# Kernel tuning notes

Hardware: AMD Instinct MI355X
Metric: run time of the kernel (lower is better)

Reference implementation:

```python
import jax, jax.numpy as jnp
from jax import lax
import numpy as np

B, S, D, H2, V = 1024, 256, 128, 5, 50257
EPS = 1e-5


def setup_inputs() -> dict:
    key = jax.random.key(0)
    ks = jax.random.split(key, 12)
    s = 0.08  # init scale ~ 1/sqrt(D)
    return {
        "x": jax.random.randint(ks[0], (B, S), 0, V),
        "emb": jax.random.normal(ks[1], (V, D), jnp.float32) * s,
        "W_ih1": jax.random.normal(ks[2], (D, D), jnp.float32) * s,
        "b_ih1": jax.random.normal(ks[3], (D,), jnp.float32) * s,
        "W_hh1": jax.random.normal(ks[4], (D, D), jnp.float32) * s,
        "b_hh1": jax.random.normal(ks[5], (D,), jnp.float32) * s,
        "g1": jnp.ones((D,), jnp.float32),
        "be1": jnp.zeros((D,), jnp.float32),
        "W_ih2": jax.random.normal(ks[6], (H2, D), jnp.float32) * s,
        "b_ih2": jax.random.normal(ks[7], (H2,), jnp.float32) * s,
        "W_hh2": jax.random.normal(ks[8], (H2, H2), jnp.float32) * s,
        "b_hh2": jax.random.normal(ks[9], (H2,), jnp.float32) * s,
        "g2": jnp.ones((H2,), jnp.float32),
        "be2": jnp.zeros((H2,), jnp.float32),
    }


def _rnn(xproj, W_hh):
    """Vanilla tanh RNN. xproj: [B,S,H] = x @ W_ih^T + b_ih + b_hh (precomputed)."""
    h0 = jnp.zeros((xproj.shape[0], W_hh.shape[0]), xproj.dtype)

    def step(h, xt):  # xt: [B,H]
        h = jnp.tanh(xt + h @ W_hh.T)
        return h, h

    _, hs = lax.scan(step, h0, jnp.swapaxes(xproj, 0, 1))  # [S,B,H]
    return jnp.swapaxes(hs, 0, 1)  # [B,S,H]


def _ln(z, g, b):
    m = jnp.mean(z, axis=-1, keepdims=True)
    v = jnp.mean(jnp.square(z - m), axis=-1, keepdims=True)
    return (z - m) * lax.rsqrt(v + EPS) * g + b


def reference(x, emb, W_ih1, b_ih1, W_hh1, b_hh1, g1, be1,
              W_ih2, b_ih2, W_hh2, b_hh2, g2, be2):
    e = emb[x]  # [B,S,D]
    z = _rnn(e @ W_ih1.T + (b_ih1 + b_hh1), W_hh1)
    z = _ln(z, g1, be1)
    z = _rnn(z @ W_ih2.T + (b_ih2 + b_hh2), W_hh2)  # [B,S,5]
    z = _ln(z, g2, be2)
    pooled = jnp.mean(z, axis=1)  # AvgPool1d over full seq -> [B,5]
    return jax.nn.softmax(pooled, axis=1)
```

## Files before the change

### kernel.cpp

```cpp
#include <hip/hip_runtime.h>
#include <stdint.h>

#define S_LEN 256
#define DIM   128
#define EPSL  1e-5f

typedef __bf16 bf16x8 __attribute__((ext_vector_type(8)));
typedef float  f32x4  __attribute__((ext_vector_type(4)));

__device__ __forceinline__ unsigned short f2bf_bits(float f) {
  union { float f; unsigned int u; } v; v.f = f;
  unsigned int r = v.u + 0x7fffu + ((v.u >> 16) & 1u);
  return (unsigned short)(r >> 16);
}
__device__ __forceinline__ float bf2f_bits(unsigned short b) {
  union { float f; unsigned int u; } v; v.u = ((unsigned int)b) << 16; return v.f;
}
__device__ __forceinline__ unsigned f2bf_rhu(float f) {
  return (__float_as_uint(f) + 0x8000u) >> 16;
}
__device__ __forceinline__ unsigned pack_rhu(float lo, float hi) {
  return __builtin_amdgcn_perm(__float_as_uint(hi) + 0x8000u,
                               __float_as_uint(lo) + 0x8000u, 0x07060302u);
}
__device__ __forceinline__ float tanh_fast(float x) {
  float e = __expf(2.f * x);
  return 1.f - 2.f * __builtin_amdgcn_rcpf(e + 1.f);
}

template<int CTRL>
__device__ __forceinline__ float dpp_rot_add(float v) {
  int r = __builtin_amdgcn_update_dpp(0, __float_as_int(v), CTRL, 0xF, 0xF, true);
  return v + __int_as_float(r);
}
template<int CTRL>
__device__ __forceinline__ float dpp_rot_max(float v) {
  int r = __builtin_amdgcn_update_dpp(0, __float_as_int(v), CTRL, 0xF, 0xF, true);
  return fmaxf(v, __int_as_float(r));
}
__device__ __forceinline__ float dpp_sum16(float v) {
  v = dpp_rot_add<0x124>(v); v = dpp_rot_add<0x128>(v);
  v = dpp_rot_add<0x39>(v);  v = dpp_rot_add<0x4E>(v);
  return v;
}
__device__ __forceinline__ float dpp_max16(float v) {
  v = dpp_rot_max<0x124>(v); v = dpp_rot_max<0x128>(v);
  v = dpp_rot_max<0x39>(v);  v = dpp_rot_max<0x4E>(v);
  return v;
}
template<int CTRL>
__device__ __forceinline__ void red_level7(float& s, float& sq, float* d) {
  s  = dpp_rot_add<CTRL>(s);
  sq = dpp_rot_add<CTRL>(sq);
#pragma unroll
  for (int j = 0; j < 5; j++) d[j] = dpp_rot_add<CTRL>(d[j]);
}
template<int JJ>
__device__ __forceinline__ float bcast16(float v) {
  int r = __builtin_amdgcn_ds_swizzle(__float_as_int(v), (JJ << 5) | 0x10);
  return __int_as_float(r);
}

union Frag8 { unsigned short us[8]; bf16x8 v; int4 i4; };

__global__ __launch_bounds__(512, 2)
void rnn_fused(const int* __restrict__ x, const float* __restrict__ emb,
               const float* __restrict__ Wih1, const float* __restrict__ bih1,
               const float* __restrict__ Whh1, const float* __restrict__ bhh1,
               const float* __restrict__ g1, const float* __restrict__ be1,
               const float* __restrict__ Wih2, const float* __restrict__ bih2,
               const float* __restrict__ Whh2, const float* __restrict__ bhh2,
               const float* __restrict__ g2, const float* __restrict__ be2,
               float* __restrict__ out)
{
  __shared__ __align__(16) unsigned short h_bf[2][16 * 128];
  __shared__ __align__(16) unsigned short e_bf[2][16 * 128];
  __shared__ int x_tile[16 * 256];

  const int tid  = threadIdx.x;
  const int wave = tid >> 6;
  const int lane = tid & 63;
  const int r0   = blockIdx.x * 16;
  const int l15  = lane & 15;
  const int q    = lane >> 4;

  for (int i = tid; i < 16 * 256; i += 512)
    x_tile[i] = x[(size_t)(r0 + (i >> 8)) * S_LEN + (i & 255)];
  for (int i = tid; i < 16 * 128; i += 512) h_bf[1][i] = 0;

  const int n1 = wave * 16 + l15;
  const float bias1v = bih1[n1] + bhh1[n1];
  bf16x8 wh[4], wih[4];
#pragma unroll
  for (int kt = 0; kt < 4; kt++) {
    int k0 = kt * 32 + q * 8;
    Frag8 fh, fa;
#pragma unroll
    for (int j = 0; j < 8; j++) {
      fh.us[j] = f2bf_bits(Whh1[n1 * DIM + k0 + j]);
      fa.us[j] = f2bf_bits(Wih1[n1 * DIM + k0 + j]);
    }
    wh[kt] = fh.v; wih[kt] = fa.v;
  }

  const bool ln_role = (wave < 4);
  float w2g[5][8], Gs[5], Bs[5], wrow[5];
  float t2_l = 0.f, g2_l = 0.f, be2_l = 0.f, validf = 0.f;
  float h2rep[5], pool_l = 0.f;
  int myrow = 0;
  float pf[2][8];
  const int gm   = (wave & 3) * 4 + q;
  const int goct = l15;
  const int gdst = gm * 128 + ((goct ^ gm) & 15) * 8;

  if (ln_role) {
    myrow = wave * 4 + q;
    int coct = (l15 ^ myrow) & 15;
#pragma unroll
    for (int j = 0; j < 8; j++) {
      int c = coct * 8 + j;
      float gc = g1[c];
#pragma unroll
      for (int jj = 0; jj < 5; jj++) w2g[jj][j] = Wih2[jj * DIM + c] * gc;
    }
#pragma unroll
    for (int jj = 0; jj < 5; jj++) { Gs[jj] = 0.f; Bs[jj] = 0.f; }
    for (int c = 0; c < DIM; c++) {
      float gc = g1[c], bc = be1[c];
#pragma unroll
      for (int jj = 0; jj < 5; jj++) {
        float w = Wih2[jj * DIM + c];
        Gs[jj] += w * gc; Bs[jj] += w * bc;
      }
    }
    validf = (l15 < 5) ? 1.f : 0.f;
    if (l15 < 5) {
      t2_l = bih2[l15] + bhh2[l15];
      g2_l = g2[l15]; be2_l = be2[l15];
#pragma unroll
      for (int jj = 0; jj < 5; jj++) wrow[jj] = Whh2[l15 * 5 + jj];
    } else {
#pragma unroll
      for (int jj = 0; jj < 5; jj++) wrow[jj] = 0.f;
    }
#pragma unroll
    for (int jj = 0; jj < 5; jj++) h2rep[jj] = 0.f;
  }
  __syncthreads();

  if (!ln_role) {
    float ta[8], tb[8];
    { int xid = x_tile[gm * 256 + 0];
      const float* pe = emb + (size_t)xid * DIM + goct * 8;
#pragma unroll
      for (int j = 0; j < 8; j++) ta[j] = pe[j]; }
    { int xid = x_tile[gm * 256 + 1];
      const float* pe = emb + (size_t)xid * DIM + goct * 8;
#pragma unroll
      for (int j = 0; j < 8; j++) tb[j] = pe[j]; }
    { int xid = x_tile[gm * 256 + 2];
      const float* pe = emb + (size_t)xid * DIM + goct * 8;
#pragma unroll
      for (int j = 0; j < 8; j++) pf[0][j] = pe[j]; }
    { int xid = x_tile[gm * 256 + 3];
      const float* pe = emb + (size_t)xid * DIM + goct * 8;
#pragma unroll
      for (int j = 0; j < 8; j++) pf[1][j] = pe[j]; }
    Frag8 pa, pb;
#pragma unroll
    for (int j = 0; j < 8; j++) { pa.us[j] = f2bf_bits(ta[j]); pb.us[j] = f2bf_bits(tb[j]); }
    *(int4*)&e_bf[0][gdst] = pa.i4;
    *(int4*)&e_bf[1][gdst] = pb.i4;
  }
  __syncthreads();

  f32x4 xpacc = {bias1v, bias1v, bias1v, bias1v};
#pragma unroll
  for (int kt = 0; kt < 4; kt++) {
    int sw = (((kt * 4 + q) ^ l15) & 15) * 8;
    bf16x8 ae = *(const bf16x8*)&e_bf[0][l15 * 128 + sw];
    xpacc = __builtin_amdgcn_mfma_f32_16x16x32_bf16(ae, wih[kt], xpacc, 0, 0, 0);
  }
  asm volatile("s_waitcnt lgkmcnt(0)\n\ts_barrier" ::: "memory");

#pragma unroll 2
  for (int t = 0; t <= S_LEN; t++) {
    f32x4 acc = xpacc;
    if (t < S_LEN) {
      const int rb = (t + 1) & 1;
#pragma unroll
      for (int kt = 0; kt < 4; kt++) {
        int sw = (((kt * 4 + q) ^ l15) & 15) * 8;
        bf16x8 ahf = *(const bf16x8*)&h_bf[rb][l15 * 128 + sw];
        acc = __builtin_amdgcn_mfma_f32_16x16x32_bf16(ahf, wh[kt], acc, 0, 0, 0);
      }
      const int wb = t & 1;
      const int c = n1;
      const int oct = c >> 3;
#pragma unroll
      for (int r = 0; r < 4; r++) {
        int row = q * 4 + r;
        h_bf[wb][row * 128 + ((oct ^ row) & 15) * 8 + (c & 7)] =
            (unsigned short)f2bf_rhu(tanh_fast(acc[r]));
      }
    }

    if (t + 1 < S_LEN) {
      f32x4 a = {bias1v, bias1v, bias1v, bias1v};
#pragma unroll
      for (int kt = 0; kt < 4; kt++) {
        int sw = (((kt * 4 + q) ^ l15) & 15) * 8;
        bf16x8 ae = *(const bf16x8*)&e_bf[(t + 1) & 1][l15 * 128 + sw];
        a = __builtin_amdgcn_mfma_f32_16x16x32_bf16(ae, wih[kt], a, 0, 0, 0);
      }
      xpacc = a;
    }

    if (!ln_role) {
      if (t + 2 < S_LEN) {
        int4 pk;
        pk.x = pack_rhu(pf[t & 1][0], pf[t & 1][1]);
        pk.y = pack_rhu(pf[t & 1][2], pf[t & 1][3]);
        pk.z = pack_rhu(pf[t & 1][4], pf[t & 1][5]);
        pk.w = pack_rhu(pf[t & 1][6], pf[t & 1][7]);
        *(int4*)&e_bf[t & 1][gdst] = pk;
      }
      if (t + 4 < S_LEN) {
        int xid = x_tile[gm * 256 + t + 4];
        const float* pe = emb + (size_t)xid * DIM + goct * 8;
#pragma unroll
        for (int j = 0; j < 8; j++) pf[t & 1][j] = pe[j];
      }
    } else if (t >= 1) {
      const int hb = (t - 1) & 1;
      Frag8 hr;
      hr.i4 = *(const int4*)&h_bf[hb][myrow * 128 + l15 * 8];
      float s = 0.f, sq = 0.f, d[5] = {0, 0, 0, 0, 0};
#pragma unroll
      for (int j = 0; j < 8; j++) {
        float v = bf2f_bits(hr.us[j]);
        s += v; sq += v * v;
#pragma unroll
        for (int jj = 0; jj < 5; jj++) d[jj] = fmaf(w2g[jj][j], v, d[jj]);
      }
      red_level7<0x124>(s, sq, d);
      red_level7<0x128>(s, sq, d);
      red_level7<0x39>(s, sq, d);
      red_level7<0x4E>(s, sq, d);
      float mean = s * (1.f / 128.f);
      float var  = sq * (1.f / 128.f) - mean * mean;
      float rstd = rsqrtf(var + EPSL);
      float p[5];
#pragma unroll
      for (int jj = 0; jj < 5; jj++)
        p[jj] = rstd * (d[jj] - mean * Gs[jj]) + Bs[jj];
      float psel = (l15 == 0) ? p[0] : (l15 == 1) ? p[1] :
                   (l15 == 2) ? p[2] : (l15 == 3) ? p[3] : p[4];
      float a = psel + t2_l;
#pragma unroll
      for (int jj = 0; jj < 5; jj++) a = fmaf(wrow[jj], h2rep[jj], a);
      float xn = tanh_fast(a);
      float s2 = dpp_sum16(xn * validf) * 0.2f;
      float dd = xn - s2;
      float v2 = dpp_sum16(dd * dd * validf) * 0.2f;
      float r2 = rsqrtf(v2 + EPSL);
      pool_l += dd * r2 * g2_l + be2_l;
      h2rep[0] = bcast16<0>(xn); h2rep[1] = bcast16<1>(xn);
      h2rep[2] = bcast16<2>(xn); h2rep[3] = bcast16<3>(xn);
      h2rep[4] = bcast16<4>(xn);
    }
    asm volatile("s_waitcnt lgkmcnt(0)\n\ts_barrier" ::: "memory");
  }

  if (ln_role) {
    float lg = pool_l * (1.f / 256.f);
    float mx = dpp_max16((l15 < 5) ? lg : -3.0e38f);
    float e  = (l15 < 5) ? __expf(lg - mx) : 0.f;
    float sm = dpp_sum16(e);
    if (l15 < 5) out[(size_t)(r0 + myrow) * 5 + l15] = e / sm;
  }
}

extern "C" void kernel_launch(void* const* d_in, const int* in_sizes, int n_in,
                              void* d_out, int out_size, void* d_ws, size_t ws_size,
                              hipStream_t stream) {
  (void)in_sizes; (void)n_in; (void)d_ws; (void)ws_size; (void)out_size;
  rnn_fused<<<dim3(64), dim3(512), 0, stream>>>(
      (const int*)  d_in[0],  (const float*)d_in[1],  (const float*)d_in[2],
      (const float*)d_in[3],  (const float*)d_in[4],  (const float*)d_in[5],
      (const float*)d_in[6],  (const float*)d_in[7],  (const float*)d_in[8],
      (const float*)d_in[9],  (const float*)d_in[10], (const float*)d_in[11],
      (const float*)d_in[12], (const float*)d_in[13], (float*)d_out);
}
```

Before: 281.3 us.

## Give every wave half-wave gather and LN/layer-2 duties instead of wave-level roles

Previously waves 0-3 ran LayerNorm and the second RNN for four rows each while waves 4-7 gathered embeddings. Now every wave handles two rows: lanes 0-31 do both the embedding gather/pack and the LN/layer-2 step, and lanes 32-63 sit idle in those sections. The aim is to shorten the critical path between barriers by splitting the per-step serial side work evenly across all eight waves. The cost is that the gather and LN phases now run back to back within each wave instead of in parallel on separate waves, and half of each wave is masked off during them.

```diff
diff --git a/kernel.cpp b/kernel.cpp
--- a/kernel.cpp
+++ b/kernel.cpp
@@ -83,6 +83,7 @@
   const int r0   = blockIdx.x * 16;
   const int l15  = lane & 15;
   const int q    = lane >> 4;
+  const bool side = (lane < 32);
 
   for (int i = tid; i < 16 * 256; i += 512)
     x_tile[i] = x[(size_t)(r0 + (i >> 8)) * S_LEN + (i & 255)];
@@ -103,18 +104,14 @@
     wh[kt] = fh.v; wih[kt] = fa.v;
   }
 
-  const bool ln_role = (wave < 4);
+  const int myrow = 2 * wave + (q & 1);
+  const int gdst  = myrow * 128 + ((l15 ^ myrow) & 15) * 8;
   float w2g[5][8], Gs[5], Bs[5], wrow[5];
   float t2_l = 0.f, g2_l = 0.f, be2_l = 0.f, validf = 0.f;
   float h2rep[5], pool_l = 0.f;
-  int myrow = 0;
   float pf[2][8];
-  const int gm   = (wave & 3) * 4 + q;
-  const int goct = l15;
-  const int gdst = gm * 128 + ((goct ^ gm) & 15) * 8;
-
-  if (ln_role) {
-    myrow = wave * 4 + q;
+
+  if (side) {
     int coct = (l15 ^ myrow) & 15;
 #pragma unroll
     for (int j = 0; j < 8; j++) {
@@ -148,22 +145,22 @@
   }
   __syncthreads();
 
-  if (!ln_role) {
+  if (side) {
     float ta[8], tb[8];
-    { int xid = x_tile[gm * 256 + 0];
-      const float* pe = emb + (size_t)xid * DIM + goct * 8;
+    { int xid = x_tile[myrow * 256 + 0];
+      const float* pe = emb + (size_t)xid * DIM + l15 * 8;
 #pragma unroll
       for (int j = 0; j < 8; j++) ta[j] = pe[j]; }
-    { int xid = x_tile[gm * 256 + 1];
-      const float* pe = emb + (size_t)xid * DIM + goct * 8;
+    { int xid = x_tile[myrow * 256 + 1];
+      const float* pe = emb + (size_t)xid * DIM + l15 * 8;
 #pragma unroll
       for (int j = 0; j < 8; j++) tb[j] = pe[j]; }
-    { int xid = x_tile[gm * 256 + 2];
-      const float* pe = emb + (size_t)xid * DIM + goct * 8;
+    { int xid = x_tile[myrow * 256 + 2];
+      const float* pe = emb + (size_t)xid * DIM + l15 * 8;
 #pragma unroll
       for (int j = 0; j < 8; j++) pf[0][j] = pe[j]; }
-    { int xid = x_tile[gm * 256 + 3];
-      const float* pe = emb + (size_t)xid * DIM + goct * 8;
+    { int xid = x_tile[myrow * 256 + 3];
+      const float* pe = emb + (size_t)xid * DIM + l15 * 8;
 #pragma unroll
       for (int j = 0; j < 8; j++) pf[1][j] = pe[j]; }
     Frag8 pa, pb;
@@ -195,12 +192,11 @@
         acc = __builtin_amdgcn_mfma_f32_16x16x32_bf16(ahf, wh[kt], acc, 0, 0, 0);
       }
       const int wb = t & 1;
-      const int c = n1;
-      const int oct = c >> 3;
+      const int oct = n1 >> 3;
 #pragma unroll
       for (int r = 0; r < 4; r++) {
         int row = q * 4 + r;
-        h_bf[wb][row * 128 + ((oct ^ row) & 15) * 8 + (c & 7)] =
+        h_bf[wb][row * 128 + ((oct ^ row) & 15) * 8 + (n1 & 7)] =
             (unsigned short)f2bf_rhu(tanh_fast(acc[r]));
       }
     }
@@ -216,7 +212,7 @@
       xpacc = a;
     }
 
-    if (!ln_role) {
+    if (side) {
       if (t + 2 < S_LEN) {
         int4 pk;
         pk.x = pack_rhu(pf[t & 1][0], pf[t & 1][1]);
@@ -226,53 +222,54 @@
         *(int4*)&e_bf[t & 1][gdst] = pk;
       }
       if (t + 4 < S_LEN) {
-        int xid = x_tile[gm * 256 + t + 4];
-        const float* pe = emb + (size_t)xid * DIM + goct * 8;
+        int xid = x_tile[myrow * 256 + t + 4];
+        const float* pe = emb + (size_t)xid * DIM + l15 * 8;
 #pragma unroll
         for (int j = 0; j < 8; j++) pf[t & 1][j] = pe[j];
       }
-    } else if (t >= 1) {
-      const int hb = (t - 1) & 1;
-      Frag8 hr;
-      hr.i4 = *(const int4*)&h_bf[hb][myrow * 128 + l15 * 8];
-      float s = 0.f, sq = 0.f, d[5] = {0, 0, 0, 0, 0};
-#pragma unroll
-      for (int j = 0; j < 8; j++) {
-        float v = bf2f_bits(hr.us[j]);
-        s += v; sq += v * v;
-#pragma unroll
-        for (int jj = 0; jj < 5; jj++) d[jj] = fmaf(w2g[jj][j], v, d[jj]);
-      }
-      red_level7<0x124>(s, sq, d);
-      red_level7<0x128>(s, sq, d);
-      red_level7<0x39>(s, sq, d);
-      red_level7<0x4E>(s, sq, d);
-      float mean = s * (1.f / 128.f);
-      float var  = sq * (1.f / 128.f) - mean * mean;
-      float rstd = rsqrtf(var + EPSL);
-      float p[5];
-#pragma unroll
-      for (int jj = 0; jj < 5; jj++)
-        p[jj] = rstd * (d[jj] - mean * Gs[jj]) + Bs[jj];
-      float psel = (l15 == 0) ? p[0] : (l15 == 1) ? p[1] :
-                   (l15 == 2) ? p[2] : (l15 == 3) ? p[3] : p[4];
-      float a = psel + t2_l;
-#pragma unroll
-      for (int jj = 0; jj < 5; jj++) a = fmaf(wrow[jj], h2rep[jj], a);
-      float xn = tanh_fast(a);
-      float s2 = dpp_sum16(xn * validf) * 0.2f;
-      float dd = xn - s2;
-      float v2 = dpp_sum16(dd * dd * validf) * 0.2f;
-      float r2 = rsqrtf(v2 + EPSL);
-      pool_l += dd * r2 * g2_l + be2_l;
-      h2rep[0] = bcast16<0>(xn); h2rep[1] = bcast16<1>(xn);
-      h2rep[2] = bcast16<2>(xn); h2rep[3] = bcast16<3>(xn);
-      h2rep[4] = bcast16<4>(xn);
+      if (t >= 1) {
+        const int hb = (t - 1) & 1;
+        Frag8 hr;
+        hr.i4 = *(const int4*)&h_bf[hb][myrow * 128 + l15 * 8];
+        float s = 0.f, sq = 0.f, d[5] = {0, 0, 0, 0, 0};
+#pragma unroll
+        for (int j = 0; j < 8; j++) {
+          float v = bf2f_bits(hr.us[j]);
+          s += v; sq += v * v;
+#pragma unroll
+          for (int jj = 0; jj < 5; jj++) d[jj] = fmaf(w2g[jj][j], v, d[jj]);
+        }
+        red_level7<0x124>(s, sq, d);
+        red_level7<0x128>(s, sq, d);
+        red_level7<0x39>(s, sq, d);
+        red_level7<0x4E>(s, sq, d);
+        float mean = s * (1.f / 128.f);
+        float var  = sq * (1.f / 128.f) - mean * mean;
+        float rstd = rsqrtf(var + EPSL);
+        float p[5];
+#pragma unroll
+        for (int jj = 0; jj < 5; jj++)
+          p[jj] = rstd * (d[jj] - mean * Gs[jj]) + Bs[jj];
+        float psel = (l15 == 0) ? p[0] : (l15 == 1) ? p[1] :
+                     (l15 == 2) ? p[2] : (l15 == 3) ? p[3] : p[4];
+        float a = psel + t2_l;
+#pragma unroll
+        for (int jj = 0; jj < 5; jj++) a = fmaf(wrow[jj], h2rep[jj], a);
+        float xn = tanh_fast(a);
+        float s2 = dpp_sum16(xn * validf) * 0.2f;
+        float dd = xn - s2;
+        float v2 = dpp_sum16(dd * dd * validf) * 0.2f;
+        float r2 = rsqrtf(v2 + EPSL);
+        pool_l += dd * r2 * g2_l + be2_l;
+        h2rep[0] = bcast16<0>(xn); h2rep[1] = bcast16<1>(xn);
+        h2rep[2] = bcast16<2>(xn); h2rep[3] = bcast16<3>(xn);
+        h2rep[4] = bcast16<4>(xn);
+      }
     }
     asm volatile("s_waitcnt lgkmcnt(0)\n\ts_barrier" ::: "memory");
   }
 
-  if (ln_role) {
+  if (side) {
     float lg = pool_l * (1.f / 256.f);
     float mx = dpp_max16((l15 < 5) ? lg : -3.0e38f);
     float e  = (l15 < 5) ? __expf(lg - mx) : 0.f;
```

Result: slower. 390.9 us (+39.0%).
